# Performance work log

Hardware: AMD Instinct MI355X
Metric: run time of the kernel (lower is better)

## Reference

```python
import jax, jax.numpy as jnp
import numpy as np

D_MODEL = 1024
D_STATE = 64
D_CONV = 4
EXPAND = 2
HEADDIM = 64
NGROUPS = 1
D_INNER = EXPAND * D_MODEL          # 2048 (= d_ssm)
NHEADS = D_INNER // HEADDIM         # 32
CONV_DIM = D_INNER + 2 * NGROUPS * D_STATE      # 2176
D_IN_PROJ = 2 * D_INNER + 2 * NGROUPS * D_STATE + NHEADS  # 4256
BATCH, SEQLEN = 1, 1024
EPS = 1e-5


def silu(x):
    return x * jax.nn.sigmoid(x)


def _causal_dwconv(xBC, conv_w, conv_b):
    # xBC: (B, L, C); conv_w: (C, W) depthwise; causal padding W-1 on the left
    x = jnp.transpose(xBC, (0, 2, 1))  # (B, C, L)
    y = jax.lax.conv_general_dilated(
        x, conv_w[:, None, :], window_strides=(1,),
        padding=[(conv_w.shape[-1] - 1, 0)],
        feature_group_count=x.shape[1])
    return jnp.transpose(y, (0, 2, 1)) + conv_b


def _mamba_dir(u, W_in, conv_w, conv_b, dt_bias, A_log, D, norm_w, W_out):
    B, L, _ = u.shape
    H, P, G, N = NHEADS, HEADDIM, NGROUPS, D_STATE
    zxbcdt = u @ W_in.T                               # (B, L, D_IN_PROJ)
    z = zxbcdt[..., :D_INNER]
    xBC = zxbcdt[..., D_INNER:D_INNER + CONV_DIM]
    dt = zxbcdt[..., -H:]
    xBC = silu(_causal_dwconv(xBC, conv_w, conv_b))
    x = xBC[..., :D_INNER].reshape(B, L, H, P)
    Bm = xBC[..., D_INNER:D_INNER + G * N].reshape(B, L, G, N)
    Cm = xBC[..., D_INNER + G * N:].reshape(B, L, G, N)
    dt = jax.nn.softplus(dt + dt_bias)                # (B, L, H)
    A = -jnp.exp(A_log.astype(jnp.float32))           # (H,)
    rep = H // G
    Bh = jnp.repeat(Bm, rep, axis=2)                  # (B, L, H, N)
    Ch = jnp.repeat(Cm, rep, axis=2)
    dA = jnp.exp(dt * A)                              # (B, L, H)
    dtx = dt[..., None] * x                           # (B, L, H, P)

    def step(h, inp):
        dA_t, dtx_t, Bh_t, Ch_t = inp                 # (B,H), (B,H,P), (B,H,N), (B,H,N)
        h = h * dA_t[..., None, None] + jnp.einsum('bhp,bhn->bhpn', dtx_t, Bh_t)
        y = jnp.einsum('bhpn,bhn->bhp', h, Ch_t)
        return h, y

    h0 = jnp.zeros((B, H, P, N), dtype=u.dtype)
    inputs = (dA.swapaxes(0, 1), dtx.swapaxes(0, 1),
              Bh.swapaxes(0, 1), Ch.swapaxes(0, 1))
    _, ys = jax.lax.scan(step, h0, inputs)            # ys: (L, B, H, P)
    y = ys.swapaxes(0, 1) + D[None, None, :, None] * x
    y = y.reshape(B, L, D_INNER)
    # gated RMSNorm (norm_before_gate=False): norm(y * silu(z)), group = d_ssm/ngroups
    yg = y * silu(z)
    yg = yg.reshape(B, L, G, -1)
    yg = yg * jax.lax.rsqrt(jnp.mean(yg * yg, axis=-1, keepdims=True) + EPS)
    yg = yg.reshape(B, L, D_INNER) * norm_w
    return yg @ W_out.T                               # (B, L, d_model)


def _forward(u, W_in_f, W_in_b, conv_w_f, conv_b_f, conv_w_b, conv_b_b,
             dt_bias_f, dt_bias_b, A_log_f, A_log_b, D_f, D_b,
             norm_w_f, norm_w_b, W_out_f, W_out_b, W_out):
    out_f = _mamba_dir(u, W_in_f, conv_w_f, conv_b_f, dt_bias_f, A_log_f,
                       D_f, norm_w_f, W_out_f)
    ub = jnp.flip(u, axis=1)
    out_b = _mamba_dir(ub, W_in_b, conv_w_b, conv_b_b, dt_bias_b, A_log_b,
                       D_b, norm_w_b, W_out_b)
    out = silu(jnp.concatenate([out_f, jnp.flip(out_b, axis=1)], axis=-1))
    return out @ W_out.T


def setup_inputs() -> dict:
    key = jax.random.key(0)
    ks = jax.random.split(key, 20)
    s = 0.02

    def dt_init(k):
        dt = jnp.exp(jax.random.uniform(k, (NHEADS,)) *
                     (np.log(0.1) - np.log(0.001)) + np.log(0.001))
        return dt + jnp.log(-jnp.expm1(-dt))  # inverse softplus

    def a_init(k):
        return jnp.log(jax.random.uniform(k, (NHEADS,), minval=1.0, maxval=16.0))

    return {
        'u': jax.random.normal(ks[0], (BATCH, SEQLEN, D_MODEL), jnp.float32),
        'W_in_f': jax.random.normal(ks[1], (D_IN_PROJ, D_MODEL), jnp.float32) * s,
        'W_in_b': jax.random.normal(ks[2], (D_IN_PROJ, D_MODEL), jnp.float32) * s,
        'conv_w_f': jax.random.normal(ks[3], (CONV_DIM, D_CONV), jnp.float32) * 0.2,
        'conv_b_f': jnp.zeros((CONV_DIM,), jnp.float32),
        'conv_w_b': jax.random.normal(ks[4], (CONV_DIM, D_CONV), jnp.float32) * 0.2,
        'conv_b_b': jnp.zeros((CONV_DIM,), jnp.float32),
        'dt_bias_f': dt_init(ks[5]),
        'dt_bias_b': dt_init(ks[6]),
        'A_log_f': a_init(ks[7]),
        'A_log_b': a_init(ks[8]),
        'D_f': jnp.ones((NHEADS,), jnp.float32),
        'D_b': jnp.ones((NHEADS,), jnp.float32),
        'norm_w_f': jnp.ones((D_INNER,), jnp.float32),
        'norm_w_b': jnp.ones((D_INNER,), jnp.float32),
        'W_out_f': jax.random.normal(ks[9], (D_MODEL, D_INNER), jnp.float32) * s,
        'W_out_b': jax.random.normal(ks[10], (D_MODEL, D_INNER), jnp.float32) * s,
        'W_out': jax.random.normal(ks[11], (D_MODEL, 2 * D_MODEL), jnp.float32) * s,
    }


def reference(u, W_in_f, W_in_b, conv_w_f, conv_b_f, conv_w_b, conv_b_b,
              dt_bias_f, dt_bias_b, A_log_f, A_log_b, D_f, D_b,
              norm_w_f, norm_w_b, W_out_f, W_out_b, W_out):
    return _forward(u, W_in_f, W_in_b, conv_w_f, conv_b_f, conv_w_b, conv_b_b,
                    dt_bias_f, dt_bias_b, A_log_f, A_log_b, D_f, D_b,
                    norm_w_f, norm_w_b, W_out_f, W_out_b, W_out)
```

## Files before the change

### kernel.cpp

```cpp
#include <hip/hip_runtime.h>
#include <hip/hip_bf16.h>
#include <stdint.h>

#define LSEQ   1024
#define DINNER 2048
#define CONVD  2176
#define LDP    4352
#define NH     32
#define HD     64
#define NST    64
#define CHUNK  64
#define NCH    16
#define LDT    72

#define POFF_CWF  0
#define POFF_CBF  8704
#define POFF_CWB  10880
#define POFF_CBB  19584
#define POFF_DTBF 21760
#define POFF_DTBB 21792
#define POFF_ALF  21824
#define POFF_ALB  21856
#define POFF_DF   21888
#define POFF_DB   21920
#define POFF_NWF  21952
#define POFF_NWB  24000
#define PTOT      26048

typedef short v8s __attribute__((ext_vector_type(8)));
typedef short v4s __attribute__((ext_vector_type(4)));
typedef float v4f __attribute__((ext_vector_type(4)));
using bf16 = __hip_bfloat16;

__device__ __forceinline__ float loadf(const void* p, size_t i, int isbf) {
    return isbf ? __bfloat162float(((const bf16*)p)[i]) : ((const float*)p)[i];
}
__device__ __forceinline__ float s2f(short s) {
    unsigned u = ((unsigned)(unsigned short)s) << 16; float f;
    __builtin_memcpy(&f, &u, 4); return f;
}
__device__ __forceinline__ short f2s(float f) {
    bf16 b = __float2bfloat16(f); short s;
    __builtin_memcpy(&s, &b, 2); return s;
}
__device__ __forceinline__ void load8(const void* p, size_t i, int isbf, float* o) {
    if (isbf) {
        v8s s = *(const v8s*)((const short*)p + i);
        #pragma unroll
        for (int e = 0; e < 8; e++) o[e] = s2f(s[e]);
    } else {
        float4 a = *(const float4*)((const float*)p + i);
        float4 b = *(const float4*)((const float*)p + i + 4);
        o[0] = a.x; o[1] = a.y; o[2] = a.z; o[3] = a.w;
        o[4] = b.x; o[5] = b.y; o[6] = b.z; o[7] = b.w;
    }
}
__device__ __forceinline__ v8s pack8(const float* o) {
    v8s r;
    #pragma unroll
    for (int e = 0; e < 8; e++) r[e] = f2s(o[e]);
    return r;
}

__device__ __forceinline__ void gload16(const bf16* g, bf16* l) {
    __builtin_amdgcn_global_load_lds(
        (const __attribute__((address_space(1))) void*)g,
        (__attribute__((address_space(3))) void*)l, 16, 0, 0);
}

template<int V> __device__ __forceinline__ void vwait() {
    if constexpr (V == 0) asm volatile("s_waitcnt vmcnt(0)" ::: "memory");
    else if constexpr (V == 3) asm volatile("s_waitcnt vmcnt(3)" ::: "memory");
    else if constexpr (V == 4) asm volatile("s_waitcnt vmcnt(4)" ::: "memory");
    else if constexpr (V == 6) asm volatile("s_waitcnt vmcnt(6)" ::: "memory");
    else if constexpr (V == 8) asm volatile("s_waitcnt vmcnt(8)" ::: "memory");
}

__global__ void detect_dtype(const unsigned int* __restrict__ nw, int* __restrict__ flag)
{
    if (threadIdx.x == 0 && blockIdx.x == 0)
        *flag = (nw[0] == 0x3F803F80u) ? 1 : 0;
}

__global__ void conv_params(const void* cwf, const void* cbf, const void* cwb, const void* cbb,
                            const void* dtbf, const void* dtbb, const void* alf, const void* alb,
                            const void* df, const void* db, const void* nwf, const void* nwb,
                            float* __restrict__ P, const int* __restrict__ flag)
{
    int idx = blockIdx.x * 256 + threadIdx.x;
    if (idx >= PTOT) return;
    int f = *flag;
    float v;
    if      (idx < POFF_CBF)  v = loadf(cwf,  idx,              f);
    else if (idx < POFF_CWB)  v = loadf(cbf,  idx - POFF_CBF,   f);
    else if (idx < POFF_CBB)  v = loadf(cwb,  idx - POFF_CWB,   f);
    else if (idx < POFF_DTBF) v = loadf(cbb,  idx - POFF_CBB,   f);
    else if (idx < POFF_DTBB) v = loadf(dtbf, idx - POFF_DTBF,  f);
    else if (idx < POFF_ALF)  v = loadf(dtbb, idx - POFF_DTBB,  f);
    else if (idx < POFF_ALB)  v = loadf(alf,  idx - POFF_ALF,   f);
    else if (idx < POFF_DF)   v = loadf(alb,  idx - POFF_ALB,   f);
    else if (idx < POFF_DB)   v = loadf(df,   idx - POFF_DF,    f);
    else if (idx < POFF_NWF)  v = loadf(db,   idx - POFF_DB,    f);
    else if (idx < POFF_NWB)  v = loadf(nwf,  idx - POFF_NWF,   f);
    else                      v = loadf(nwb,  idx - POFF_NWB,   f);
    P[idx] = v;
}

#define NPU  262144
#define NPW  1114112
#define NWO  786432
__global__ void prep_all(const void* __restrict__ U, const void* __restrict__ Wf, const void* __restrict__ Wb,
                         const void* __restrict__ Wof, const void* __restrict__ Wob, const void* __restrict__ Wom,
                         bf16* __restrict__ Au, bf16* __restrict__ Wp,
                         bf16* __restrict__ Woc, bf16* __restrict__ Wo2, const int* __restrict__ flag)
{
    int idx = blockIdx.x * 256 + threadIdx.x;
    int f = *flag;
    if (idx < NPU) {
        int r = idx >> 7, c8 = (idx & 127) * 8;
        int src = (r < 1024) ? r : (2047 - r);
        float o[8]; load8(U, (size_t)src * 1024 + c8, f, o);
        *(v8s*)(Au + (size_t)r * 1024 + c8) = pack8(o);
    } else if (idx < NPU + NPW) {
        int j = idx - NPU;
        int r = (j >> 7) % 4352;
        int d = j / (4352 * 128);
        int c8 = (j & 127) * 8;
        float o[8] = {0.f, 0.f, 0.f, 0.f, 0.f, 0.f, 0.f, 0.f};
        if (r < 4256) load8(d ? Wb : Wf, (size_t)r * 1024 + c8, f, o);
        *(v8s*)(Wp + (size_t)j * 8) = pack8(o);
    } else if (idx < NPU + NPW + NWO) {
        int j = idx - NPU - NPW;
        int seg = j / 262144;
        size_t j8 = (size_t)(j % 262144) * 8;
        float o[8];
        if (seg == 0)      { load8(Wof, j8, f, o); *(v8s*)(Woc + j8) = pack8(o); }
        else if (seg == 1) { load8(Wob, j8, f, o); *(v8s*)(Woc + 1024 * 2048 + j8) = pack8(o); }
        else               { load8(Wom, j8, f, o); *(v8s*)(Wo2 + j8) = pack8(o); }
    }
}

template<int BM, int BN, int BK>
__global__ __launch_bounds__(256) void gemm_bt(
    const bf16* __restrict__ A, const bf16* __restrict__ B0, const bf16* __restrict__ B1,
    int rowSplit, void* __restrict__ Cv, int M, int N, int K, const int* outFlag,
    int epi, int swzMode)
{
    constexpr int RPL = 2048 / BK;
    constexpr int AN  = BM / RPL;
    constexpr int BNN = BN / RPL;
    constexpr int LPS = AN + BNN;
    constexpr int MI  = BM / 32;
    constexpr int NJ  = BN / 32;
    constexpr int KS  = BK / 32;
    constexpr int CPR = BK / 8;
    __shared__ __align__(16) bf16 LdsA[4][BM * BK];
    __shared__ __align__(16) bf16 LdsB[4][BN * BK];
    const int tid  = threadIdx.x;
    const int lane = tid & 63;
    const int wave = tid >> 6;
    const int quad = lane >> 4, l16 = lane & 15;
    const int wrow = (wave >> 1) * (BM / 2);
    const int wcol = (wave & 1)  * (BN / 2);

    int bx = blockIdx.x, by = blockIdx.y;
    if (swzMode >= 0) {
        const int gx = gridDim.x, gy = gridDim.y;
        const int nwg = gx * gy;
        const int cpx = nwg >> 3;
        const int p   = by * gx + bx;
        const int L   = (p & 7) * cpx + (p >> 3);
        if (swzMode) { by = L % gy; bx = L / gy; }
        else         { bx = L % gx; by = L / gx; }
    }
    const int m0 = by * BM;
    const int n0 = bx * BN;
    const bf16* Bp = (m0 >= rowSplit) ? B1 : B0;
    const int mode = (outFlag && !epi) ? *outFlag : 1;

    const int r0 = tid / CPR;
    const int pc = tid % CPR;
    const int fx_w = (BK == 32) ? ((r0 >> 1) & 3) : (r0 & 7);
    const int csw = (pc ^ fx_w) * 8;
    const bf16* gA[AN];
    const bf16* gB[BNN];
    #pragma unroll
    for (int a = 0; a < AN; a++)  gA[a] = A  + (size_t)(m0 + r0 + RPL * a) * K + csw;
    #pragma unroll
    for (int q = 0; q < BNN; q++) gB[q] = Bp + (size_t)(n0 + r0 + RPL * q) * K + csw;

    v4f acc[MI][NJ];
    #pragma unroll
    for (int i = 0; i < MI; i++)
        #pragma unroll
        for (int j = 0; j < NJ; j++) acc[i][j] = (v4f){0.f, 0.f, 0.f, 0.f};

    const int nt = K / BK;

    auto STAGE = [&](int buf, int t) {
        const int k0 = t * BK;
        #pragma unroll
        for (int a = 0; a < AN; a++)
            gload16(gA[a] + k0, &LdsA[buf][a * 2048 + tid * 8]);
        #pragma unroll
        for (int q = 0; q < BNN; q++)
            gload16(gB[q] + k0, &LdsB[buf][q * 2048 + tid * 8]);
    };

    STAGE(0, 0);
    STAGE(1, 1);
    STAGE(2, 2);

    for (int t = 0; t < nt; ++t) {
        const int buf = t & 3;
        if (t < nt - 2)       vwait<2 * LPS>();
        else if (t == nt - 2) vwait<LPS>();
        else                  vwait<0>();
        __builtin_amdgcn_s_barrier();
        if (t + 3 < nt) STAGE((t + 3) & 3, t + 3);

        const bf16* as = &LdsA[buf][0];
        const bf16* bs = &LdsB[buf][0];
        #pragma unroll
        for (int ks = 0; ks < KS; ks++) {
            v8s af[MI], bfr[NJ];
            #pragma unroll
            for (int i = 0; i < MI; i++) {
                int row = wrow + i * 16 + l16;
                int fx = (BK == 32) ? ((row >> 1) & 3) : (row & 7);
                af[i] = *(const v8s*)&as[row * BK + (((ks * 4 + quad) ^ fx)) * 8];
            }
            #pragma unroll
            for (int j = 0; j < NJ; j++) {
                int row = wcol + j * 16 + l16;
                int fx = (BK == 32) ? ((row >> 1) & 3) : (row & 7);
                bfr[j] = *(const v8s*)&bs[row * BK + (((ks * 4 + quad) ^ fx)) * 8];
            }
            #pragma unroll
            for (int i = 0; i < MI; i++)
                #pragma unroll
                for (int j = 0; j < NJ; j++)
                    acc[i][j] = __builtin_amdgcn_mfma_f32_16x16x32_bf16(af[i], bfr[j], acc[i][j], 0, 0, 0);
        }
    }

    #pragma unroll
    for (int i = 0; i < MI; i++) {
        int row = m0 + wrow + i * 16 + quad * 4;
        #pragma unroll
        for (int j = 0; j < NJ; j++) {
            int col = n0 + wcol + j * 16 + l16;
            if (epi) {
                bf16* Act = (bf16*)Cv;
                #pragma unroll
                for (int r = 0; r < 4; r++) {
                    float x = acc[i][j][r];
                    float v = x / (1.f + __expf(-x));
                    int rr = row + r;
                    if (rr < 1024) Act[(size_t)rr * 2048 + col] = __float2bfloat16(v);
                    else           Act[(size_t)(2047 - rr) * 2048 + 1024 + col] = __float2bfloat16(v);
                }
            } else if (mode) {
                bf16* C = (bf16*)Cv;
                #pragma unroll
                for (int r = 0; r < 4; r++)
                    C[(size_t)(row + r) * N + col] = __float2bfloat16(acc[i][j][r]);
            } else {
                float* C = (float*)Cv;
                #pragma unroll
                for (int r = 0; r < 4; r++)
                    C[(size_t)(row + r) * N + col] = acc[i][j][r];
            }
        }
    }
}

#define NCONV (2 * LSEQ * (CONVD / 8))
#define NDT   (2 * LSEQ * NH)
__global__ void conv_dt(const bf16* __restrict__ Z, const float* __restrict__ P,
                        bf16* __restrict__ XC, float* __restrict__ DT, float* __restrict__ LDA)
{
    int idx = blockIdx.x * 256 + threadIdx.x;
    if (idx < NCONV) {
        int c8 = (idx % (CONVD / 8)) * 8;
        int l = (idx / (CONVD / 8)) % LSEQ;
        int d = idx / ((CONVD / 8) * LSEQ);
        const float* w    = P + (d ? POFF_CWB : POFF_CWF) + c8 * 4;
        const float* bias = P + (d ? POFF_CBB : POFF_CBF) + c8;
        const bf16* zbase = Z + ((size_t)(d * LSEQ + l)) * LDP + DINNER + c8;
        float s[8];
        #pragma unroll
        for (int e = 0; e < 8; e++) s[e] = bias[e];
        #pragma unroll
        for (int k = 0; k < 4; k++) {
            int ls = l - 3 + k;
            if (ls >= 0) {
                v8s zv = *(const v8s*)(zbase + (ls - l) * LDP);
                #pragma unroll
                for (int e = 0; e < 8; e++) s[e] += w[e * 4 + k] * s2f(zv[e]);
            }
        }
        float o[8];
        #pragma unroll
        for (int e = 0; e < 8; e++) o[e] = s[e] / (1.f + __expf(-s[e]));
        *(v8s*)(XC + (size_t)(d * LSEQ + l) * CONVD + c8) = pack8(o);
    } else if (idx < NCONV + NDT) {
        int j = idx - NCONV;
        int h = j & 31; int l = (j >> 5) & (LSEQ - 1); int d = j >> 15;
        float raw = s2f(((const short*)Z)[((size_t)(d * LSEQ + l)) * LDP + DINNER + CONVD + h])
                  + P[POFF_DTBF + d * 32 + h];
        float dt = (raw > 20.f) ? raw : log1pf(__expf(raw));
        float Aa = -__expf(P[POFF_ALF + d * 32 + h]);
        DT[j] = dt;
        LDA[j] = Aa * dt;
    }
}

__global__ __launch_bounds__(256) void ssd_intra(const bf16* __restrict__ XC,
                                                 const float* __restrict__ DT,
                                                 const float* __restrict__ LDA,
                                                 float* __restrict__ Y, float* __restrict__ S,
                                                 float* __restrict__ Pdec, float* __restrict__ LSg)
{
    __shared__ __align__(16) short sB [64 * LDT];
    __shared__ __align__(16) short sBT[64 * LDT];
    __shared__ __align__(16) short sC [64 * LDT];
    __shared__ __align__(16) short sXT[64 * LDT];
    __shared__ __align__(16) short sGW[64 * LDT];
    __shared__ float sls[64], sdt[64], sW[64];

    int b = blockIdx.x;
    int d = b >> 9, h = (b >> 4) & 31, c = b & 15;
    int r0 = c * CHUNK;
    int t = threadIdx.x;
    const bf16* base = XC + (size_t)d * LSEQ * CONVD;

    {
        int l = t >> 2, nb = (t & 3) * 16;
        const bf16* row = base + (size_t)(r0 + l) * CONVD;
        const short* Brow = (const short*)(row + DINNER) + nb;
        const short* Crow = (const short*)(row + DINNER + NST) + nb;
        const short* Xrow = (const short*)(row + h * HD) + nb;
        v8s b0 = *(const v8s*)Brow, b1 = *(const v8s*)(Brow + 8);
        v8s c0 = *(const v8s*)Crow, c1 = *(const v8s*)(Crow + 8);
        v8s x0 = *(const v8s*)Xrow, x1 = *(const v8s*)(Xrow + 8);
        *(v8s*)&sB[l * LDT + nb]     = b0;
        *(v8s*)&sB[l * LDT + nb + 8] = b1;
        *(v8s*)&sC[l * LDT + nb]     = c0;
        *(v8s*)&sC[l * LDT + nb + 8] = c1;
        #pragma unroll
        for (int k = 0; k < 8; k++) {
            sBT[(nb + k)     * LDT + l] = b0[k];
            sBT[(nb + 8 + k) * LDT + l] = b1[k];
            sXT[(nb + k)     * LDT + l] = x0[k];
            sXT[(nb + 8 + k) * LDT + l] = x1[k];
        }
    }
    if (t < 64) {
        size_t ofs = (size_t)d * LSEQ * NH + (size_t)(r0 + t) * NH + h;
        float v = LDA[ofs];
        float dtv = DT[ofs];
        #pragma unroll
        for (int off = 1; off < 64; off <<= 1) {
            float u = __shfl_up(v, off);
            if (t >= off) v += u;
        }
        sls[t] = v; sdt[t] = dtv;
        float ls63 = __shfl(v, 63);
        sW[t] = __expf(ls63 - v) * dtv;
        LSg[(size_t)b * 64 + t] = v;
        if (t == 63) Pdec[b] = __expf(v);
    }
    __syncthreads();

    int lane = t & 63, wave = t >> 6;
    int quad = lane >> 4, l16 = lane & 15;

    {
        v8s a0 = *(const v8s*)&sC[(wave * 16 + l16) * LDT + quad * 8];
        v8s a1 = *(const v8s*)&sC[(wave * 16 + l16) * LDT + quad * 8 + 32];
        #pragma unroll
        for (int jt = 0; jt < 4; jt++) {
            v8s b0 = *(const v8s*)&sB[(jt * 16 + l16) * LDT + quad * 8];
            v8s b1 = *(const v8s*)&sB[(jt * 16 + l16) * LDT + quad * 8 + 32];
            v4f acc = (v4f){0.f, 0.f, 0.f, 0.f};
            acc = __builtin_amdgcn_mfma_f32_16x16x32_bf16(a0, b0, acc, 0, 0, 0);
            acc = __builtin_amdgcn_mfma_f32_16x16x32_bf16(a1, b1, acc, 0, 0, 0);
            #pragma unroll
            for (int r = 0; r < 4; r++) {
                int ii = wave * 16 + quad * 4 + r;
                int jj = jt * 16 + l16;
                float wgt = (jj <= ii) ? __expf(sls[ii] - sls[jj]) * sdt[jj] : 0.f;
                sGW[ii * LDT + jj] = f2s(acc[r] * wgt);
            }
        }
    }
    __syncthreads();

    float* ybase = Y + ((size_t)d * LSEQ + r0) * DINNER + h * HD;

    {
        v8s a0 = *(const v8s*)&sGW[(wave * 16 + l16) * LDT + quad * 8];
        v8s a1 = *(const v8s*)&sGW[(wave * 16 + l16) * LDT + quad * 8 + 32];
        #pragma unroll
        for (int pt = 0; pt < 4; pt++) {
            v8s b0 = *(const v8s*)&sXT[(pt * 16 + l16) * LDT + quad * 8];
            v8s b1 = *(const v8s*)&sXT[(pt * 16 + l16) * LDT + quad * 8 + 32];
            v4f acc = (v4f){0.f, 0.f, 0.f, 0.f};
            acc = __builtin_amdgcn_mfma_f32_16x16x32_bf16(a0, b0, acc, 0, 0, 0);
            acc = __builtin_amdgcn_mfma_f32_16x16x32_bf16(a1, b1, acc, 0, 0, 0);
            #pragma unroll
            for (int r = 0; r < 4; r++) {
                int ii = wave * 16 + quad * 4 + r;
                int p  = pt * 16 + l16;
                ybase[(size_t)ii * DINNER + p] = acc[r];
            }
        }
    }

    {
        v8s a0r = *(const v8s*)&sXT[(wave * 16 + l16) * LDT + quad * 8];
        v8s a1r = *(const v8s*)&sXT[(wave * 16 + l16) * LDT + quad * 8 + 32];
        v8s a0, a1;
        #pragma unroll
        for (int e = 0; e < 8; e++) {
            a0[e] = f2s(s2f(a0r[e]) * sW[quad * 8 + e]);
            a1[e] = f2s(s2f(a1r[e]) * sW[quad * 8 + 32 + e]);
        }
        float* sout = S + (size_t)b * 4096;
        #pragma unroll
        for (int nt = 0; nt < 4; nt++) {
            v8s b0 = *(const v8s*)&sBT[(nt * 16 + l16) * LDT + quad * 8];
            v8s b1 = *(const v8s*)&sBT[(nt * 16 + l16) * LDT + quad * 8 + 32];
            v4f acc = (v4f){0.f, 0.f, 0.f, 0.f};
            acc = __builtin_amdgcn_mfma_f32_16x16x32_bf16(a0, b0, acc, 0, 0, 0);
            acc = __builtin_amdgcn_mfma_f32_16x16x32_bf16(a1, b1, acc, 0, 0, 0);
            #pragma unroll
            for (int r = 0; r < 4; r++) {
                int p = wave * 16 + quad * 4 + r;
                int n = nt * 16 + l16;
                sout[p * 64 + n] = acc[r];
            }
        }
    }
}

__global__ __launch_bounds__(256) void scan2(float* __restrict__ S, const float* __restrict__ Pdec)
{
    int b = blockIdx.x;
    int off = blockIdx.y * 1024 + threadIdx.x * 4;
    float4 H = make_float4(0.f, 0.f, 0.f, 0.f);
    for (int c = 0; c < NCH; c++) {
        float* so = S + (((size_t)b * 16 + c) * 4096) + off;
        float4 sc = *(const float4*)so;
        float Pc = Pdec[b * 16 + c];
        *(float4*)so = H;
        H.x = H.x * Pc + sc.x;
        H.y = H.y * Pc + sc.y;
        H.z = H.z * Pc + sc.z;
        H.w = H.w * Pc + sc.w;
    }
}

__global__ __launch_bounds__(256) void ssd_inter(const bf16* __restrict__ XC,
                                                 const float* __restrict__ Hin,
                                                 const float* __restrict__ LSg,
                                                 float* __restrict__ Y)
{
    __shared__ __align__(16) short sH [64 * LDT];
    __shared__ __align__(16) short sCk[64 * LDT];
    __shared__ float sEls[64];

    int b = blockIdx.x;
    int d = b >> 9, h = (b >> 4) & 31, c = b & 15;
    int r0 = c * CHUNK;
    int t = threadIdx.x;
    const bf16* base = XC + (size_t)d * LSEQ * CONVD;
    {
        int l = t >> 2, nb = (t & 3) * 16;
        const float* hrow = Hin + (size_t)b * 4096 + l * 64 + nb;
        const short* crow = (const short*)(base + (size_t)(r0 + l) * CONVD + DINNER + NST) + nb;
        v8s c0 = *(const v8s*)crow, c1 = *(const v8s*)(crow + 8);
        *(v8s*)&sCk[l * LDT + nb]     = c0;
        *(v8s*)&sCk[l * LDT + nb + 8] = c1;
        #pragma unroll
        for (int k = 0; k < 16; k += 4) {
            float4 vh = *(const float4*)(hrow + k);
            v4s hv; hv[0] = f2s(vh.x); hv[1] = f2s(vh.y); hv[2] = f2s(vh.z); hv[3] = f2s(vh.w);
            *(v4s*)&sH[l * LDT + nb + k] = hv;
        }
    }
    if (t < 64) sEls[t] = __expf(LSg[(size_t)b * 64 + t]);
    __syncthreads();

    int lane = t & 63, wave = t >> 6;
    int quad = lane >> 4, l16 = lane & 15;
    float* ybase = Y + ((size_t)d * LSEQ + r0) * DINNER + h * HD;

    v8s a0 = *(const v8s*)&sCk[(wave * 16 + l16) * LDT + quad * 8];
    v8s a1 = *(const v8s*)&sCk[(wave * 16 + l16) * LDT + quad * 8 + 32];
    #pragma unroll
    for (int pt = 0; pt < 4; pt++) {
        v8s b0 = *(const v8s*)&sH[(pt * 16 + l16) * LDT + quad * 8];
        v8s b1 = *(const v8s*)&sH[(pt * 16 + l16) * LDT + quad * 8 + 32];
        v4f acc = (v4f){0.f, 0.f, 0.f, 0.f};
        acc = __builtin_amdgcn_mfma_f32_16x16x32_bf16(a0, b0, acc, 0, 0, 0);
        acc = __builtin_amdgcn_mfma_f32_16x16x32_bf16(a1, b1, acc, 0, 0, 0);
        #pragma unroll
        for (int r = 0; r < 4; r++) {
            int ii = wave * 16 + quad * 4 + r;
            int p  = pt * 16 + l16;
            ybase[(size_t)ii * DINNER + p] += sEls[ii] * acc[r];
        }
    }
}

__global__ __launch_bounds__(256) void gate_norm(const float* __restrict__ Y, const bf16* __restrict__ XC,
                                                 const bf16* __restrict__ Z, const float* __restrict__ P,
                                                 bf16* __restrict__ YG)
{
    int rowi = blockIdx.x;
    int d = rowi >> 10;
    int tid = threadIdx.x;
    const float* yrow = Y + (size_t)rowi * DINNER;
    const bf16* xrow = XC + (size_t)rowi * CONVD;
    const bf16* zrow = Z + (size_t)rowi * LDP;
    const float* Dv = P + POFF_DF + d * 32;
    const float* nw = P + POFF_NWF + d * 2048;
    int j0 = tid * 8;
    float Dh = Dv[j0 >> 6];
    float4 ya = *(const float4*)(yrow + j0), yb = *(const float4*)(yrow + j0 + 4);
    v8s xv8 = *(const v8s*)(xrow + j0);
    v8s zv = *(const v8s*)(zrow + j0);
    float yv[8] = {ya.x, ya.y, ya.z, ya.w, yb.x, yb.y, yb.z, yb.w};
    float g[8]; float ss = 0.f;
    #pragma unroll
    for (int e = 0; e < 8; e++) {
        float y = yv[e] + Dh * s2f(xv8[e]);
        float z = s2f(zv[e]);
        float gg = y * (z / (1.f + __expf(-z)));
        g[e] = gg; ss += gg * gg;
    }
    #pragma unroll
    for (int off = 32; off; off >>= 1) ss += __shfl_xor(ss, off);
    __shared__ float red[4];
    if ((tid & 63) == 0) red[tid >> 6] = ss;
    __syncthreads();
    float tot = red[0] + red[1] + red[2] + red[3];
    float scale = rsqrtf(tot * (1.f / 2048.f) + 1e-5f);
    float o[8];
    #pragma unroll
    for (int e = 0; e < 8; e++) o[e] = g[e] * scale * nw[j0 + e];
    *(v8s*)(YG + (size_t)rowi * DINNER + j0) = pack8(o);
}

extern "C" void kernel_launch(void* const* d_in, const int* in_sizes, int n_in,
                              void* d_out, int out_size, void* d_ws, size_t ws_size,
                              hipStream_t stream)
{
    const void* u      = d_in[0];
    const void* Winf   = d_in[1];
    const void* Winb   = d_in[2];
    const void* convwf = d_in[3];
    const void* convbf = d_in[4];
    const void* convwb = d_in[5];
    const void* convbb = d_in[6];
    const void* dtbf   = d_in[7];
    const void* dtbb   = d_in[8];
    const void* Alf    = d_in[9];
    const void* Alb    = d_in[10];
    const void* Dfv    = d_in[11];
    const void* Dbv    = d_in[12];
    const void* nwf    = d_in[13];
    const void* nwb    = d_in[14];
    const void* Woutf  = d_in[15];
    const void* Woutb  = d_in[16];
    const void* Wout   = d_in[17];

    char* w = (char*)d_ws;
    int*   flag = (int*)w;   w += 256;
    bf16*  Au   = (bf16*)w;
    w += (size_t)2048 * 1024 * 2;
    bf16*  Wp   = (bf16*)w;
    float* Y    = (float*)w; w += (size_t)2 * 4352 * 1024 * 2;
    bf16*  Woc  = (bf16*)w;
    bf16*  Act  = (bf16*)w;  w += (size_t)2 * 1024 * 2048 * 2;
    bf16*  Wo2  = (bf16*)w;  w += (size_t)1024 * 2048 * 2;
    float* P    = (float*)w; w += 104448;
    bf16*  Zb   = (bf16*)w;  w += (size_t)2048 * 4352 * 2;
    bf16*  XC   = (bf16*)w;  w += (size_t)2048 * 2176 * 2;
    float* DT   = (float*)w; w += (size_t)2048 * 32 * 4;
    float* LDA  = (float*)w; w += (size_t)2048 * 32 * 4;
    bf16*  YG   = (bf16*)w;  w += (size_t)2048 * 2048 * 2;
    float* S    = (float*)w; w += (size_t)2 * 32 * 16 * 64 * 64 * 4;
    float* Pdec = (float*)w; w += 4096;
    float* LSg  = (float*)w; w += (size_t)2 * 32 * 16 * 64 * 4;
    if ((size_t)(w - (char*)d_ws) > ws_size) return;

    detect_dtype<<<1, 64, 0, stream>>>((const unsigned int*)nwf, flag);
    conv_params<<<(PTOT + 255) / 256, 256, 0, stream>>>(convwf, convbf, convwb, convbb,
        dtbf, dtbb, Alf, Alb, Dfv, Dbv, nwf, nwb, P, flag);
    prep_all<<<(NPU + NPW + NWO) / 256, 256, 0, stream>>>(u, Winf, Winb, Woutf, Woutb, Wout,
        Au, Wp, Woc, Wo2, flag);

    dim3 g1(4352 / 64, 2048 / 128);
    gemm_bt<128, 64, 32><<<g1, 256, 0, stream>>>(Au, Wp, Wp + (size_t)4352 * 1024, 1024,
                                                 Zb, 2048, 4352, 1024, nullptr, 0, 1);

    conv_dt<<<(NCONV + NDT + 255) / 256, 256, 0, stream>>>(Zb, P, XC, DT, LDA);

    ssd_intra<<<1024, 256, 0, stream>>>(XC, DT, LDA, Y, S, Pdec, LSg);
    scan2<<<dim3(64, 4), 256, 0, stream>>>(S, Pdec);
    ssd_inter<<<1024, 256, 0, stream>>>(XC, S, LSg, Y);

    gate_norm<<<2048, 256, 0, stream>>>(Y, XC, Zb, P, YG);

    dim3 g2(1024 / 64, 2048 / 64);
    gemm_bt<64, 64, 64><<<g2, 256, 0, stream>>>(YG, Woc, Woc + (size_t)1024 * 2048, 1024,
                                                Act, 2048, 1024, 2048, nullptr, 1, -1);

    dim3 g3(1024 / 64, 1024 / 64);
    gemm_bt<64, 64, 64><<<g3, 256, 0, stream>>>(Act, Wo2, Wo2, 1 << 30,
                                                d_out, 1024, 1024, 2048, flag, 0, -1);
}
```

Baseline: 290.8 us.

## Store SSD intermediates in bf16, split Y into separate buffers, drop dtype-detect kernel

```diff
diff --git a/kernel.cpp b/kernel.cpp
--- a/kernel.cpp
+++ b/kernel.cpp
@@ -27,6 +27,8 @@
 #define POFF_NWB  24000
 #define PTOT      26048
 
+#define BF16_ONES 0x3F803F80u
+
 typedef short v8s __attribute__((ext_vector_type(8)));
 typedef short v4s __attribute__((ext_vector_type(4)));
 typedef float v4f __attribute__((ext_vector_type(4)));
@@ -76,20 +78,15 @@
     else if constexpr (V == 8) asm volatile("s_waitcnt vmcnt(8)" ::: "memory");
 }
 
-__global__ void detect_dtype(const unsigned int* __restrict__ nw, int* __restrict__ flag)
-{
-    if (threadIdx.x == 0 && blockIdx.x == 0)
-        *flag = (nw[0] == 0x3F803F80u) ? 1 : 0;
-}
-
 __global__ void conv_params(const void* cwf, const void* cbf, const void* cwb, const void* cbb,
                             const void* dtbf, const void* dtbb, const void* alf, const void* alb,
                             const void* df, const void* db, const void* nwf, const void* nwb,
-                            float* __restrict__ P, const int* __restrict__ flag)
+                            float* __restrict__ P, int* __restrict__ flag)
 {
     int idx = blockIdx.x * 256 + threadIdx.x;
     if (idx >= PTOT) return;
-    int f = *flag;
+    int f = (((const unsigned int*)nwf)[0] == BF16_ONES) ? 1 : 0;
+    if (idx == 0) *flag = f;
     float v;
     if      (idx < POFF_CBF)  v = loadf(cwf,  idx,              f);
     else if (idx < POFF_CWB)  v = loadf(cbf,  idx - POFF_CBF,   f);
@@ -111,11 +108,12 @@
 #define NWO  786432
 __global__ void prep_all(const void* __restrict__ U, const void* __restrict__ Wf, const void* __restrict__ Wb,
                          const void* __restrict__ Wof, const void* __restrict__ Wob, const void* __restrict__ Wom,
+                         const void* __restrict__ nwf,
                          bf16* __restrict__ Au, bf16* __restrict__ Wp,
-                         bf16* __restrict__ Woc, bf16* __restrict__ Wo2, const int* __restrict__ flag)
+                         bf16* __restrict__ Woc, bf16* __restrict__ Wo2)
 {
     int idx = blockIdx.x * 256 + threadIdx.x;
-    int f = *flag;
+    int f = (((const unsigned int*)nwf)[0] == BF16_ONES) ? 1 : 0;
     if (idx < NPU) {
         int r = idx >> 7, c8 = (idx & 127) * 8;
         int src = (r < 1024) ? r : (2047 - r);
@@ -319,7 +317,7 @@
 __global__ __launch_bounds__(256) void ssd_intra(const bf16* __restrict__ XC,
                                                  const float* __restrict__ DT,
                                                  const float* __restrict__ LDA,
-                                                 float* __restrict__ Y, float* __restrict__ S,
+                                                 bf16* __restrict__ Yi, bf16* __restrict__ S,
                                                  float* __restrict__ Pdec, float* __restrict__ LSg)
 {
     __shared__ __align__(16) short sB [64 * LDT];
@@ -397,7 +395,7 @@
     }
     __syncthreads();
 
-    float* ybase = Y + ((size_t)d * LSEQ + r0) * DINNER + h * HD;
+    bf16* ybase = Yi + ((size_t)d * LSEQ + r0) * DINNER + h * HD;
 
     {
         v8s a0 = *(const v8s*)&sGW[(wave * 16 + l16) * LDT + quad * 8];
@@ -413,7 +411,7 @@
             for (int r = 0; r < 4; r++) {
                 int ii = wave * 16 + quad * 4 + r;
                 int p  = pt * 16 + l16;
-                ybase[(size_t)ii * DINNER + p] = acc[r];
+                ybase[(size_t)ii * DINNER + p] = __float2bfloat16(acc[r]);
             }
         }
     }
@@ -427,7 +425,7 @@
             a0[e] = f2s(s2f(a0r[e]) * sW[quad * 8 + e]);
             a1[e] = f2s(s2f(a1r[e]) * sW[quad * 8 + 32 + e]);
         }
-        float* sout = S + (size_t)b * 4096;
+        short* sout = (short*)S + (size_t)b * 4096;
         #pragma unroll
         for (int nt = 0; nt < 4; nt++) {
             v8s b0 = *(const v8s*)&sBT[(nt * 16 + l16) * LDT + quad * 8];
@@ -439,33 +437,34 @@
             for (int r = 0; r < 4; r++) {
                 int p = wave * 16 + quad * 4 + r;
                 int n = nt * 16 + l16;
-                sout[p * 64 + n] = acc[r];
+                sout[p * 64 + n] = f2s(acc[r]);
             }
         }
     }
 }
 
-__global__ __launch_bounds__(256) void scan2(float* __restrict__ S, const float* __restrict__ Pdec)
+__global__ __launch_bounds__(256) void scan2(bf16* __restrict__ S, const float* __restrict__ Pdec)
 {
     int b = blockIdx.x;
     int off = blockIdx.y * 1024 + threadIdx.x * 4;
-    float4 H = make_float4(0.f, 0.f, 0.f, 0.f);
+    float h0 = 0.f, h1 = 0.f, h2 = 0.f, h3 = 0.f;
     for (int c = 0; c < NCH; c++) {
-        float* so = S + (((size_t)b * 16 + c) * 4096) + off;
-        float4 sc = *(const float4*)so;
+        short* so = (short*)S + (((size_t)b * 16 + c) * 4096) + off;
+        v4s sc = *(const v4s*)so;
         float Pc = Pdec[b * 16 + c];
-        *(float4*)so = H;
-        H.x = H.x * Pc + sc.x;
-        H.y = H.y * Pc + sc.y;
-        H.z = H.z * Pc + sc.z;
-        H.w = H.w * Pc + sc.w;
+        v4s hv; hv[0] = f2s(h0); hv[1] = f2s(h1); hv[2] = f2s(h2); hv[3] = f2s(h3);
+        *(v4s*)so = hv;
+        h0 = h0 * Pc + s2f(sc[0]);
+        h1 = h1 * Pc + s2f(sc[1]);
+        h2 = h2 * Pc + s2f(sc[2]);
+        h3 = h3 * Pc + s2f(sc[3]);
     }
 }
 
 __global__ __launch_bounds__(256) void ssd_inter(const bf16* __restrict__ XC,
-                                                 const float* __restrict__ Hin,
+                                                 const bf16* __restrict__ Hin,
                                                  const float* __restrict__ LSg,
-                                                 float* __restrict__ Y)
+                                                 bf16* __restrict__ Ye)
 {
     __shared__ __align__(16) short sH [64 * LDT];
     __shared__ __align__(16) short sCk[64 * LDT];
@@ -478,24 +477,21 @@
     const bf16* base = XC + (size_t)d * LSEQ * CONVD;
     {
         int l = t >> 2, nb = (t & 3) * 16;
-        const float* hrow = Hin + (size_t)b * 4096 + l * 64 + nb;
+        const short* hrow = (const short*)Hin + (size_t)b * 4096 + l * 64 + nb;
         const short* crow = (const short*)(base + (size_t)(r0 + l) * CONVD + DINNER + NST) + nb;
+        v8s h0 = *(const v8s*)hrow, h1 = *(const v8s*)(hrow + 8);
         v8s c0 = *(const v8s*)crow, c1 = *(const v8s*)(crow + 8);
+        *(v8s*)&sH[l * LDT + nb]      = h0;
+        *(v8s*)&sH[l * LDT + nb + 8]  = h1;
         *(v8s*)&sCk[l * LDT + nb]     = c0;
         *(v8s*)&sCk[l * LDT + nb + 8] = c1;
-        #pragma unroll
-        for (int k = 0; k < 16; k += 4) {
-            float4 vh = *(const float4*)(hrow + k);
-            v4s hv; hv[0] = f2s(vh.x); hv[1] = f2s(vh.y); hv[2] = f2s(vh.z); hv[3] = f2s(vh.w);
-            *(v4s*)&sH[l * LDT + nb + k] = hv;
-        }
     }
     if (t < 64) sEls[t] = __expf(LSg[(size_t)b * 64 + t]);
     __syncthreads();
 
     int lane = t & 63, wave = t >> 6;
     int quad = lane >> 4, l16 = lane & 15;
-    float* ybase = Y + ((size_t)d * LSEQ + r0) * DINNER + h * HD;
+    bf16* ybase = Ye + ((size_t)d * LSEQ + r0) * DINNER + h * HD;
 
     v8s a0 = *(const v8s*)&sCk[(wave * 16 + l16) * LDT + quad * 8];
     v8s a1 = *(const v8s*)&sCk[(wave * 16 + l16) * LDT + quad * 8 + 32];
@@ -510,33 +506,35 @@
         for (int r = 0; r < 4; r++) {
             int ii = wave * 16 + quad * 4 + r;
             int p  = pt * 16 + l16;
-            ybase[(size_t)ii * DINNER + p] += sEls[ii] * acc[r];
-        }
-    }
-}
-
-__global__ __launch_bounds__(256) void gate_norm(const float* __restrict__ Y, const bf16* __restrict__ XC,
+            ybase[(size_t)ii * DINNER + p] = __float2bfloat16(sEls[ii] * acc[r]);
+        }
+    }
+}
+
+__global__ __launch_bounds__(256) void gate_norm(const bf16* __restrict__ Yi, const bf16* __restrict__ Ye,
+                                                 const bf16* __restrict__ XC,
                                                  const bf16* __restrict__ Z, const float* __restrict__ P,
                                                  bf16* __restrict__ YG)
 {
     int rowi = blockIdx.x;
     int d = rowi >> 10;
     int tid = threadIdx.x;
-    const float* yrow = Y + (size_t)rowi * DINNER;
+    const bf16* yirow = Yi + (size_t)rowi * DINNER;
+    const bf16* yerow = Ye + (size_t)rowi * DINNER;
     const bf16* xrow = XC + (size_t)rowi * CONVD;
     const bf16* zrow = Z + (size_t)rowi * LDP;
     const float* Dv = P + POFF_DF + d * 32;
     const float* nw = P + POFF_NWF + d * 2048;
     int j0 = tid * 8;
     float Dh = Dv[j0 >> 6];
-    float4 ya = *(const float4*)(yrow + j0), yb = *(const float4*)(yrow + j0 + 4);
+    v8s yi8 = *(const v8s*)(yirow + j0);
+    v8s ye8 = *(const v8s*)(yerow + j0);
     v8s xv8 = *(const v8s*)(xrow + j0);
     v8s zv = *(const v8s*)(zrow + j0);
-    float yv[8] = {ya.x, ya.y, ya.z, ya.w, yb.x, yb.y, yb.z, yb.w};
     float g[8]; float ss = 0.f;
     #pragma unroll
     for (int e = 0; e < 8; e++) {
-        float y = yv[e] + Dh * s2f(xv8[e]);
+        float y = s2f(yi8[e]) + s2f(ye8[e]) + Dh * s2f(xv8[e]);
         float z = s2f(zv[e]);
         float gg = y * (z / (1.f + __expf(-z)));
         g[e] = gg; ss += gg * gg;
@@ -579,10 +577,8 @@
 
     char* w = (char*)d_ws;
     int*   flag = (int*)w;   w += 256;
-    bf16*  Au   = (bf16*)w;
-    w += (size_t)2048 * 1024 * 2;
-    bf16*  Wp   = (bf16*)w;
-    float* Y    = (float*)w; w += (size_t)2 * 4352 * 1024 * 2;
+    bf16*  Au   = (bf16*)w;  w += (size_t)2048 * 1024 * 2;
+    bf16*  Wp   = (bf16*)w;  w += (size_t)2 * 4352 * 1024 * 2;
     bf16*  Woc  = (bf16*)w;
     bf16*  Act  = (bf16*)w;  w += (size_t)2 * 1024 * 2048 * 2;
     bf16*  Wo2  = (bf16*)w;  w += (size_t)1024 * 2048 * 2;
@@ -592,16 +588,17 @@
     float* DT   = (float*)w; w += (size_t)2048 * 32 * 4;
     float* LDA  = (float*)w; w += (size_t)2048 * 32 * 4;
     bf16*  YG   = (bf16*)w;  w += (size_t)2048 * 2048 * 2;
-    float* S    = (float*)w; w += (size_t)2 * 32 * 16 * 64 * 64 * 4;
+    bf16*  S    = (bf16*)w;  w += (size_t)2 * 32 * 16 * 64 * 64 * 2;
     float* Pdec = (float*)w; w += 4096;
     float* LSg  = (float*)w; w += (size_t)2 * 32 * 16 * 64 * 4;
+    bf16*  Yi   = (bf16*)w;  w += (size_t)2048 * 2048 * 2;
+    bf16*  Ye   = (bf16*)w;  w += (size_t)2048 * 2048 * 2;
     if ((size_t)(w - (char*)d_ws) > ws_size) return;
 
-    detect_dtype<<<1, 64, 0, stream>>>((const unsigned int*)nwf, flag);
     conv_params<<<(PTOT + 255) / 256, 256, 0, stream>>>(convwf, convbf, convwb, convbb,
         dtbf, dtbb, Alf, Alb, Dfv, Dbv, nwf, nwb, P, flag);
     prep_all<<<(NPU + NPW + NWO) / 256, 256, 0, stream>>>(u, Winf, Winb, Woutf, Woutb, Wout,
-        Au, Wp, Woc, Wo2, flag);
+        nwf, Au, Wp, Woc, Wo2);
 
     dim3 g1(4352 / 64, 2048 / 128);
     gemm_bt<128, 64, 32><<<g1, 256, 0, stream>>>(Au, Wp, Wp + (size_t)4352 * 1024, 1024,
@@ -609,11 +606,11 @@
 
     conv_dt<<<(NCONV + NDT + 255) / 256, 256, 0, stream>>>(Zb, P, XC, DT, LDA);
 
-    ssd_intra<<<1024, 256, 0, stream>>>(XC, DT, LDA, Y, S, Pdec, LSg);
+    ssd_intra<<<1024, 256, 0, stream>>>(XC, DT, LDA, Yi, S, Pdec, LSg);
     scan2<<<dim3(64, 4), 256, 0, stream>>>(S, Pdec);
-    ssd_inter<<<1024, 256, 0, stream>>>(XC, S, LSg, Y);
-
-    gate_norm<<<2048, 256, 0, stream>>>(Y, XC, Zb, P, YG);
+    ssd_inter<<<1024, 256, 0, stream>>>(XC, S, LSg, Ye);
+
+    gate_norm<<<2048, 256, 0, stream>>>(Yi, Ye, XC, Zb, P, YG);
 
     dim3 g2(1024 / 64, 2048 / 64);
     gemm_bt<64, 64, 64><<<g2, 256, 0, stream>>>(YG, Woc, Woc + (size_t)1024 * 2048, 1024,
```

Result: faster. 282.2 us (-3.0%).
